# Kernel tuning notes

Measured on AMD Instinct MI355X. Metric: run time of the kernel, lower is better.

Reference implementation:

```python
import jax, jax.numpy as jnp
import numpy as np
from jax.scipy.special import logsumexp

HEAD = 12
EPS = 1.0


def _sinkhorn(dots):
    # dots: [b, h, n, n]. Faithful to the torch code: eps=1, max_iter=3,
    # update order u, v, u (the err<1e-6 early-break never triggers for
    # unconverged random-scale inputs, so we unroll the 3 iterations).
    C = -dots
    b, h, n, m = C.shape
    log_mu = -jnp.log(jnp.asarray(n, dtype=C.dtype))  # log(1/n)
    log_nu = -jnp.log(jnp.asarray(m, dtype=C.dtype))
    u = jnp.zeros((b, h, n), dtype=C.dtype)
    v = jnp.zeros((b, h, m), dtype=C.dtype)

    def M(u, v):
        # (-C + u_i + v_j) / eps
        return (-C + u[..., :, None] + v[..., None, :]) / EPS

    # i = 0: row update
    u = EPS * (log_mu - logsumexp(M(u, v), axis=-1)) + u
    # i = 1: column update (logsumexp over transpose == axis=-2)
    v = EPS * (log_nu - logsumexp(M(u, v), axis=-2)) + v
    # i = 2: row update
    u = EPS * (log_mu - logsumexp(M(u, v), axis=-1)) + u
    return jnp.exp(M(u, v))


def setup_inputs() -> dict:
    key = jax.random.key(0)
    ks = jax.random.split(key, 6)
    b, n, f = 8, 1024, 768
    x = jax.random.normal(ks[0], (b, n, f), dtype=jnp.float32)
    s = 1.0 / np.sqrt(f)
    Wq = jax.random.normal(ks[1], (f, f), dtype=jnp.float32) * s
    Wk = jax.random.normal(ks[2], (f, f), dtype=jnp.float32) * s
    Wv = jax.random.normal(ks[3], (f, f), dtype=jnp.float32) * s
    Wo = jax.random.normal(ks[4], (f, f), dtype=jnp.float32) * s
    bo = jax.random.normal(ks[5], (f,), dtype=jnp.float32) * 0.01
    return {"x": x, "Wq": Wq, "Wk": Wk, "Wv": Wv, "Wo": Wo, "bo": bo}


def reference(x, Wq, Wk, Wv, Wo, bo):
    b, n, f = x.shape
    h = HEAD
    d = f // h
    scale = d ** (-0.5)
    # nn.Linear: y = x @ W.T
    q = (x @ Wq.T).reshape(b, n, h, d).transpose(0, 2, 1, 3)  # [b,h,n,d]
    k = (x @ Wk.T).reshape(b, n, h, d).transpose(0, 2, 1, 3)
    v = (x @ Wv.T).reshape(b, n, h, d).transpose(0, 2, 1, 3)
    dots = jnp.einsum("bhid,bhjd->bhij", q, k) * scale  # [b,h,n,n]
    attn = _sinkhorn(dots)
    out = jnp.einsum("bhij,bhjd->bhid", attn, v)
    out = out.transpose(0, 2, 1, 3).reshape(b, n, f)
    return out @ Wo.T + bo
```

## Files before the change

kernel.cpp:

```cpp
#include <hip/hip_runtime.h>

#define DEV __device__ __forceinline__

typedef __attribute__((ext_vector_type(4))) float f32x4;
typedef __attribute__((ext_vector_type(16))) float f32x16;
typedef __attribute__((ext_vector_type(8))) short bf16x8;

DEV short f2bf(float f) {
    union { float f; unsigned u; } v; v.f = f;
    unsigned r = (v.u + 0x7fffu + ((v.u >> 16) & 1u)) >> 16;
    return (short)r;
}

#ifndef __has_builtin
#define __has_builtin(x) 0
#endif
#if __has_builtin(__builtin_amdgcn_cvt_pk_bf16_f32)
DEV unsigned pkbf(float a, float b) {
    auto r = __builtin_amdgcn_cvt_pk_bf16_f32(a, b);
    union { __typeof__(r) v; unsigned u; } u; u.v = r; return u.u;
}
#else
DEV unsigned pkbf(float a, float b) {
    return (unsigned)(unsigned short)f2bf(a) | ((unsigned)(unsigned short)f2bf(b) << 16);
}
#endif

DEV void gl_lds16(const void* g, void* l) {
    __builtin_amdgcn_global_load_lds(
        (__attribute__((address_space(1))) void*)(g),
        (__attribute__((address_space(3))) void*)(l), 16, 0, 0);
}

template <int ITERS>
DEV void stage_tile(const short* g, int ldg, short* lds, int t) {
    const int w = t >> 6;
#pragma unroll
    for (int it = 0; it < ITERS; ++it) {
        int row = it * 32 + (t >> 3);
        int cx = (t & 7) ^ ((t >> 3) & 7);
        gl_lds16(g + row * ldg + cx * 8, (char*)lds + it * 4096 + (w << 10));
    }
}

DEV bf16x8 ldfrag(const short* lds, int r, int kc) {
    return *(const bf16x8*)(lds + r * 64 + ((kc ^ (r & 7)) << 3));
}

__global__ void cvt_all(const float* __restrict__ x,
                        const float* __restrict__ wq, const float* __restrict__ wk,
                        const float* __restrict__ wv, const float* __restrict__ wo,
                        short* __restrict__ xb,
                        short* __restrict__ wqb, short* __restrict__ wkb,
                        short* __restrict__ wvb, short* __restrict__ wob) {
    int b = blockIdx.x;
    const float* s; short* d; int i;
    if (b < 6144) {
        s = x; d = xb; i = b * 256 + threadIdx.x;
    } else {
        int r = b - 6144;
        int wi = r / 576, rem = r - wi * 576;
        s = (wi == 0) ? wq : (wi == 1) ? wk : (wi == 2) ? wv : wo;
        d = (wi == 0) ? wqb : (wi == 1) ? wkb : (wi == 2) ? wvb : wob;
        i = rem * 256 + threadIdx.x;
    }
    float4 v = ((const float4*)s)[i];
    short4 o;
    o.x = f2bf(v.x); o.y = f2bf(v.y); o.z = f2bf(v.z); o.w = f2bf(v.w);
    ((short4*)d)[i] = o;
}

#define TSTRIDE 136
__global__ __launch_bounds__(256, 3) void proj_gemm(
    const short* __restrict__ xb,
    const short* __restrict__ wq, const short* __restrict__ wk, const short* __restrict__ wv,
    short* __restrict__ Qg, short* __restrict__ Kg, short* __restrict__ Vtg)
{
    __shared__ __align__(16) char smem[40960];
    short* const At = (short*)smem;
    short* const Bq = (short*)(smem + 16384);
    short* const Bk = (short*)(smem + 24576);
    short* const Bv = (short*)(smem + 32768);
    short* const Ct = (short*)smem;
    const int t = threadIdx.x;
    const int row0 = blockIdx.x * 128, col0 = blockIdx.y * 64;
    const int lane = t & 63, w = t >> 6;
    const int l31 = lane & 31, lh = lane >> 5;
    const int wm = w >> 1, wn = w & 1;

    f32x16 acc[3][2];
#pragma unroll
    for (int z = 0; z < 3; ++z)
#pragma unroll
        for (int tm = 0; tm < 2; ++tm) acc[z][tm] = (f32x16)(0.f);

    const short* Asrc = xb + (size_t)row0 * 768;
    const short* Qs = wq + (size_t)col0 * 768;
    const short* Ks = wk + (size_t)col0 * 768;
    const short* Vs = wv + (size_t)col0 * 768;

    for (int k = 0; k < 12; ++k) {
        __syncthreads();
        stage_tile<4>(Asrc + k * 64, 768, At, t);
        stage_tile<2>(Qs + k * 64, 768, Bq, t);
        stage_tile<2>(Ks + k * 64, 768, Bk, t);
        stage_tile<2>(Vs + k * 64, 768, Bv, t);
        __syncthreads();
#pragma unroll
        for (int s = 0; s < 4; ++s) {
            bf16x8 af[2];
#pragma unroll
            for (int tm = 0; tm < 2; ++tm) af[tm] = ldfrag(At, wm * 64 + tm * 32 + l31, s * 2 + lh);
            bf16x8 b0 = ldfrag(Bq, wn * 32 + l31, s * 2 + lh);
            bf16x8 b1 = ldfrag(Bk, wn * 32 + l31, s * 2 + lh);
            bf16x8 b2 = ldfrag(Bv, wn * 32 + l31, s * 2 + lh);
#pragma unroll
            for (int tm = 0; tm < 2; ++tm) {
                acc[0][tm] = __builtin_amdgcn_mfma_f32_32x32x16_bf16(af[tm], b0, acc[0][tm], 0, 0, 0);
                acc[1][tm] = __builtin_amdgcn_mfma_f32_32x32x16_bf16(af[tm], b1, acc[1][tm], 0, 0, 0);
                acc[2][tm] = __builtin_amdgcn_mfma_f32_32x32x16_bf16(af[tm], b2, acc[2][tm], 0, 0, 0);
            }
        }
    }
    __syncthreads();

    const int bb = row0 >> 10;
    const int head = bb * 12 + (col0 >> 6);

#pragma unroll
    for (int z = 0; z < 2; ++z) {
        const float sc = (z == 0) ? 0.125f * 1.4426950408889634f : 1.0f;
        const int ddl = wn * 32 + l31;
#pragma unroll
        for (int tm = 0; tm < 2; ++tm)
#pragma unroll
            for (int reg = 0; reg < 16; ++reg) {
                int rrl = wm * 64 + tm * 32 + (reg & 3) + 8 * (reg >> 2) + 4 * lh;
                Ct[rrl * TSTRIDE + ddl] = f2bf(acc[z][tm][reg] * sc);
            }
        __syncthreads();
        short* dst = (z == 0) ? Qg : Kg;
#pragma unroll
        for (int it = 0; it < 4; ++it) {
            int row = it * 32 + (t >> 3);
            int ck = t & 7;
            bf16x8 v = *(const bf16x8*)(Ct + row * TSTRIDE + ck * 8);
            int rr = (row0 & 1023) + row;
            *(bf16x8*)(dst + ((size_t)head * 1024 + rr) * 64 + ck * 8) = v;
        }
        __syncthreads();
    }

    {
        const int ddl = wn * 32 + l31;
#pragma unroll
        for (int tm = 0; tm < 2; ++tm)
#pragma unroll
            for (int g = 0; g < 4; ++g) {
                int rrl = wm * 64 + tm * 32 + 8 * g + 4 * lh;
                int j6 = rrl & 63;
                int pp = (rrl & ~63) | (j6 & 32) | ((j6 & 12) << 1) | ((j6 & 16) >> 2);
                short4 v4;
                v4.x = f2bf(acc[2][tm][4 * g + 0]);
                v4.y = f2bf(acc[2][tm][4 * g + 1]);
                v4.z = f2bf(acc[2][tm][4 * g + 2]);
                v4.w = f2bf(acc[2][tm][4 * g + 3]);
                *(short4*)(Ct + ddl * TSTRIDE + pp) = v4;
            }
        __syncthreads();
#pragma unroll
        for (int it = 0; it < 4; ++it) {
            int row = it * 16 + (t >> 4);
            int ck = t & 15;
            bf16x8 v = *(const bf16x8*)(Ct + row * TSTRIDE + ck * 8);
            *(bf16x8*)(Vtg + ((size_t)head * 64 + row) * 1024 + (row0 & 1023) + ck * 8) = v;
        }
    }
}

__global__ __launch_bounds__(256, 5) void lse_pass(
    const short* __restrict__ Aall, const short* __restrict__ Ball,
    const float* __restrict__ bias, float* __restrict__ outv,
    float bias_sign, float out_sign)
{
    __shared__ __align__(16) short At[64 * 64];
    __shared__ __align__(16) short Bt[128 * 64];
    __shared__ __align__(16) float biasl[1024];
    const int t = threadIdx.x;
    const int head = blockIdx.x % 96;
    const int r0 = (blockIdx.x / 96) * 64;
    const int lane = t & 63, w = t >> 6, quad = lane >> 4, c = lane & 15;
    const short* A = Aall + (size_t)head * 65536;
    const short* B = Ball + (size_t)head * 65536;

    stage_tile<2>(A + r0 * 64, 64, At, t);
    if (bias) {
        float4 v = ((const float4*)(bias + (size_t)head * 1024))[t];
        v.x *= bias_sign; v.y *= bias_sign; v.z *= bias_sign; v.w *= bias_sign;
        ((float4*)biasl)[t] = v;
    } else ((float4*)biasl)[t] = make_float4(0.f, 0.f, 0.f, 0.f);

    float lsum = 0.f;
    bf16x8 bfr[2];
    bool first = true;

    for (int j0 = 0; j0 < 1024; j0 += 128) {
        __syncthreads();
        stage_tile<4>(B + j0 * 64, 64, Bt, t);
        __syncthreads();
        if (first) {
#pragma unroll
            for (int ks = 0; ks < 2; ++ks) bfr[ks] = ldfrag(At, w * 16 + c, ks * 4 + quad);
            first = false;
        }
        f32x4 sacc[8];
#pragma unroll
        for (int fm = 0; fm < 8; ++fm) {
            float4 b4 = *(const float4*)(biasl + j0 + fm * 16 + quad * 4);
            sacc[fm] = (f32x4){b4.x, b4.y, b4.z, b4.w};
        }
#pragma unroll
        for (int ks = 0; ks < 2; ++ks) {
            bf16x8 af[8];
#pragma unroll
            for (int fm = 0; fm < 8; ++fm) af[fm] = ldfrag(Bt, fm * 16 + c, ks * 4 + quad);
#pragma unroll
            for (int fm = 0; fm < 8; ++fm)
                sacc[fm] = __builtin_amdgcn_mfma_f32_16x16x32_bf16(af[fm], bfr[ks], sacc[fm], 0, 0, 0);
        }
#pragma unroll
        for (int fm = 0; fm < 8; ++fm) {
            float p0 = __builtin_amdgcn_exp2f(sacc[fm][0]);
            float p1 = __builtin_amdgcn_exp2f(sacc[fm][1]);
            float p2 = __builtin_amdgcn_exp2f(sacc[fm][2]);
            float p3 = __builtin_amdgcn_exp2f(sacc[fm][3]);
            lsum += (p0 + p1) + (p2 + p3);
        }
    }

    lsum += __shfl_xor(lsum, 16);
    lsum += __shfl_xor(lsum, 32);
    if (quad == 0)
        outv[(size_t)head * 1024 + r0 + w * 16 + c] =
            out_sign * __builtin_amdgcn_logf(lsum);
}

__global__ __launch_bounds__(256, 4) void flash_pass(
    const short* __restrict__ Qall, const short* __restrict__ Kall,
    const short* __restrict__ Vtall, const float* __restrict__ v1,
    short* __restrict__ ctx)
{
    __shared__ __align__(16) short Qt[128 * 64];
    __shared__ __align__(16) short Kt[64 * 64];
    __shared__ __align__(16) short Vtl[64 * 64];
    __shared__ __align__(16) float v1l[1024];
    const int t = threadIdx.x;
    const int head = blockIdx.x % 96;
    const int r0 = (blockIdx.x / 96) * 128;
    const int lane = t & 63, w = t >> 6, quad = lane >> 4, c = lane & 15;
    const short* Q = Qall + (size_t)head * 65536;
    const short* K = Kall + (size_t)head * 65536;
    const short* Vt = Vtall + (size_t)head * 65536;

    stage_tile<4>(Q + r0 * 64, 64, Qt, t);
    ((float4*)v1l)[t] = ((const float4*)(v1 + (size_t)head * 1024))[t];

    float lsum[2] = {0.f, 0.f};
    f32x4 oacc[4][2];
#pragma unroll
    for (int md = 0; md < 4; ++md)
#pragma unroll
        for (int ni = 0; ni < 2; ++ni) oacc[md][ni] = (f32x4){0.f, 0.f, 0.f, 0.f};

    bf16x8 qfr[2][2];
    bool first = true;

    for (int j0 = 0; j0 < 1024; j0 += 64) {
        __syncthreads();
        stage_tile<2>(K + j0 * 64, 64, Kt, t);
        stage_tile<2>(Vt + j0, 1024, Vtl, t);
        __syncthreads();
        if (first) {
#pragma unroll
            for (int fn = 0; fn < 2; ++fn)
#pragma unroll
                for (int ks = 0; ks < 2; ++ks)
                    qfr[fn][ks] = ldfrag(Qt, w * 32 + fn * 16 + c, ks * 4 + quad);
            first = false;
        }
        f32x4 sacc[4][2];
#pragma unroll
        for (int fm = 0; fm < 4; ++fm) {
            float4 b4 = *(const float4*)(v1l + j0 + fm * 16 + quad * 4);
#pragma unroll
            for (int fn = 0; fn < 2; ++fn) sacc[fm][fn] = (f32x4){b4.x, b4.y, b4.z, b4.w};
        }
#pragma unroll
        for (int ks = 0; ks < 2; ++ks) {
            bf16x8 af[4];
#pragma unroll
            for (int fm = 0; fm < 4; ++fm) af[fm] = ldfrag(Kt, fm * 16 + c, ks * 4 + quad);
#pragma unroll
            for (int fm = 0; fm < 4; ++fm)
#pragma unroll
                for (int fn = 0; fn < 2; ++fn)
                    sacc[fm][fn] = __builtin_amdgcn_mfma_f32_16x16x32_bf16(af[fm], qfr[fn][ks], sacc[fm][fn], 0, 0, 0);
        }
        unsigned pk[4][2][2];
#pragma unroll
        for (int fm = 0; fm < 4; ++fm)
#pragma unroll
            for (int fn = 0; fn < 2; ++fn) {
                float p0 = __builtin_amdgcn_exp2f(sacc[fm][fn][0]);
                float p1 = __builtin_amdgcn_exp2f(sacc[fm][fn][1]);
                float p2 = __builtin_amdgcn_exp2f(sacc[fm][fn][2]);
                float p3 = __builtin_amdgcn_exp2f(sacc[fm][fn][3]);
                lsum[fn] += (p0 + p1) + (p2 + p3);
                pk[fm][fn][0] = pkbf(p0, p1);
                pk[fm][fn][1] = pkbf(p2, p3);
            }
#pragma unroll
        for (int ks = 0; ks < 2; ++ks) {
            bf16x8 vaf[4];
#pragma unroll
            for (int md = 0; md < 4; ++md) vaf[md] = ldfrag(Vtl, md * 16 + c, ks * 4 + quad);
#pragma unroll
            for (int ni = 0; ni < 2; ++ni) {
                union { bf16x8 v8; unsigned u4[4]; } b;
                b.u4[0] = pk[2 * ks + 0][ni][0];
                b.u4[1] = pk[2 * ks + 0][ni][1];
                b.u4[2] = pk[2 * ks + 1][ni][0];
                b.u4[3] = pk[2 * ks + 1][ni][1];
#pragma unroll
                for (int md = 0; md < 4; ++md)
                    oacc[md][ni] = __builtin_amdgcn_mfma_f32_16x16x32_bf16(vaf[md], b.v8, oacc[md][ni], 0, 0, 0);
            }
        }
    }

#pragma unroll
    for (int fn = 0; fn < 2; ++fn) {
        float s = lsum[fn];
        s += __shfl_xor(s, 16); s += __shfl_xor(s, 32);
        lsum[fn] = s;
    }
    const int bb = head / 12, hh = head % 12;
#pragma unroll
    for (int ni = 0; ni < 2; ++ni) {
        float nrm = __builtin_amdgcn_rcpf(1024.f * lsum[ni]);
        int rr = r0 + w * 32 + ni * 16 + c;
#pragma unroll
        for (int md = 0; md < 4; ++md) {
            short4 v4;
            v4.x = f2bf(oacc[md][ni][0] * nrm);
            v4.y = f2bf(oacc[md][ni][1] * nrm);
            v4.z = f2bf(oacc[md][ni][2] * nrm);
            v4.w = f2bf(oacc[md][ni][3] * nrm);
            *(short4*)(ctx + ((size_t)(bb * 1024 + rr)) * 768 + hh * 64 + md * 16 + quad * 4) = v4;
        }
    }
}

__global__ __launch_bounds__(256, 4) void out_gemm(
    const short* __restrict__ ctxb, const short* __restrict__ wo,
    const float* __restrict__ bo, float* __restrict__ out)
{
    __shared__ __align__(16) short At[128 * 64];
    __shared__ __align__(16) short Bt[128 * 64];
    const int t = threadIdx.x;
    const int row0 = blockIdx.x * 128, col0 = blockIdx.y * 128;
    const int lane = t & 63, w = t >> 6;
    const int l31 = lane & 31, lh = lane >> 5;
    const int wm = w >> 1, wn = w & 1;

    f32x16 acc[2][2];
#pragma unroll
    for (int i = 0; i < 2; ++i)
#pragma unroll
        for (int j = 0; j < 2; ++j) acc[i][j] = (f32x16)(0.f);

    for (int k0 = 0; k0 < 768; k0 += 64) {
        __syncthreads();
        stage_tile<4>(ctxb + (size_t)row0 * 768 + k0, 768, At, t);
        stage_tile<4>(wo + (size_t)col0 * 768 + k0, 768, Bt, t);
        __syncthreads();
#pragma unroll
        for (int s = 0; s < 4; ++s) {
            bf16x8 af[2], bfr[2];
#pragma unroll
            for (int tm = 0; tm < 2; ++tm) af[tm] = ldfrag(At, wm * 64 + tm * 32 + l31, s * 2 + lh);
#pragma unroll
            for (int tn = 0; tn < 2; ++tn) bfr[tn] = ldfrag(Bt, wn * 64 + tn * 32 + l31, s * 2 + lh);
#pragma unroll
            for (int tm = 0; tm < 2; ++tm)
#pragma unroll
                for (int tn = 0; tn < 2; ++tn)
                    acc[tm][tn] = __builtin_amdgcn_mfma_f32_32x32x16_bf16(af[tm], bfr[tn], acc[tm][tn], 0, 0, 0);
        }
    }
#pragma unroll
    for (int tm = 0; tm < 2; ++tm)
#pragma unroll
        for (int tn = 0; tn < 2; ++tn) {
            int gc = col0 + wn * 64 + tn * 32 + l31;
            float b = bo[gc];
#pragma unroll
            for (int reg = 0; reg < 16; ++reg) {
                int gr = row0 + wm * 64 + tm * 32 + (reg & 3) + 8 * (reg >> 2) + 4 * lh;
                out[(size_t)gr * 768 + gc] = acc[tm][tn][reg] + b;
            }
        }
}

extern "C" void kernel_launch(void* const* d_in, const int* in_sizes, int n_in,
                              void* d_out, int out_size, void* d_ws, size_t ws_size,
                              hipStream_t stream) {
    const float* x  = (const float*)d_in[0];
    const float* Wq = (const float*)d_in[1];
    const float* Wk = (const float*)d_in[2];
    const float* Wv = (const float*)d_in[3];
    const float* Wo = (const float*)d_in[4];
    const float* bo = (const float*)d_in[5];
    float* out = (float*)d_out;

    char* p = (char*)d_ws;
    short* xb  = (short*)p; p += (size_t)8192 * 768 * 2;
    short* wqb = (short*)p; p += (size_t)768 * 768 * 2;
    short* wkb = (short*)p; p += (size_t)768 * 768 * 2;
    short* wvb = (short*)p; p += (size_t)768 * 768 * 2;
    short* wob = (short*)p; p += (size_t)768 * 768 * 2;
    short* Qg  = (short*)p; p += (size_t)96 * 1024 * 64 * 2;
    short* Kg  = (short*)p; p += (size_t)96 * 1024 * 64 * 2;
    short* Vtg = (short*)p; p += (size_t)96 * 1024 * 64 * 2;
    float* r1  = (float*)p; p += (size_t)96 * 1024 * 4;
    float* v1  = (float*)p; p += (size_t)96 * 1024 * 4;
    short* ctx = (short*)p; p += (size_t)8192 * 768 * 2;

    cvt_all<<<6144 + 4 * 576, 256, 0, stream>>>(x, Wq, Wk, Wv, Wo, xb, wqb, wkb, wvb, wob);

    proj_gemm<<<dim3(64, 12), 256, 0, stream>>>(xb, wqb, wkb, wvb, Qg, Kg, Vtg);

    lse_pass<<<1536, 256, 0, stream>>>(Qg, Kg, nullptr, r1, 0.f, 1.f);
    lse_pass<<<1536, 256, 0, stream>>>(Kg, Qg, r1, v1, -1.f, -1.f);

    flash_pass<<<768, 256, 0, stream>>>(Qg, Kg, Vtg, v1, ctx);

    out_gemm<<<dim3(64, 6), 256, 0, stream>>>(ctx, wob, bo, out);
}
```

Baseline: 224.6 us.

## Switch attention passes to 32x32x16 MFMA and double LSE row tile

Rewrites lse_pass and flash_pass to use 32x32x16 bf16 MFMA instructions instead of 16x16x32, with one 32-row query tile per wave. lse_pass now processes 128 rows per block (half the grid) so each staged B tile is reused across more rows. The V^T permutation in proj_gemm is changed to match the new P-fragment layout for the PV MFMA. The aim is fewer LDS fragment loads per FLOP and fewer cross-lane reductions, at the cost of larger accumulators, lower lse occupancy and a smaller grid.

Measured after the change: 211.0 us. 6.1% less time.

```diff
diff --git a/kernel.cpp b/kernel.cpp
--- a/kernel.cpp
+++ b/kernel.cpp
@@ -158,8 +158,7 @@
 #pragma unroll
             for (int g = 0; g < 4; ++g) {
                 int rrl = wm * 64 + tm * 32 + 8 * g + 4 * lh;
-                int j6 = rrl & 63;
-                int pp = (rrl & ~63) | (j6 & 32) | ((j6 & 12) << 1) | ((j6 & 16) >> 2);
+                int pp = (rrl & ~12) | ((rrl & 8) >> 1) | ((rrl & 4) << 1);
                 short4 v4;
                 v4.x = f2bf(acc[2][tm][4 * g + 0]);
                 v4.y = f2bf(acc[2][tm][4 * g + 1]);
@@ -178,22 +177,23 @@
     }
 }
 
-__global__ __launch_bounds__(256, 5) void lse_pass(
+__global__ __launch_bounds__(256, 4) void lse_pass(
     const short* __restrict__ Aall, const short* __restrict__ Ball,
     const float* __restrict__ bias, float* __restrict__ outv,
     float bias_sign, float out_sign)
 {
-    __shared__ __align__(16) short At[64 * 64];
+    __shared__ __align__(16) short At[128 * 64];
     __shared__ __align__(16) short Bt[128 * 64];
     __shared__ __align__(16) float biasl[1024];
     const int t = threadIdx.x;
     const int head = blockIdx.x % 96;
-    const int r0 = (blockIdx.x / 96) * 64;
-    const int lane = t & 63, w = t >> 6, quad = lane >> 4, c = lane & 15;
+    const int r0 = (blockIdx.x / 96) * 128;
+    const int lane = t & 63, w = t >> 6;
+    const int l31 = lane & 31, lh = lane >> 5;
     const short* A = Aall + (size_t)head * 65536;
     const short* B = Ball + (size_t)head * 65536;
 
-    stage_tile<2>(A + r0 * 64, 64, At, t);
+    stage_tile<4>(A + r0 * 64, 64, At, t);
     if (bias) {
         float4 v = ((const float4*)(bias + (size_t)head * 1024))[t];
         v.x *= bias_sign; v.y *= bias_sign; v.z *= bias_sign; v.w *= bias_sign;
@@ -201,7 +201,7 @@
     } else ((float4*)biasl)[t] = make_float4(0.f, 0.f, 0.f, 0.f);
 
     float lsum = 0.f;
-    bf16x8 bfr[2];
+    bf16x8 bfr[4];
     bool first = true;
 
     for (int j0 = 0; j0 < 1024; j0 += 128) {
@@ -210,38 +210,42 @@
         __syncthreads();
         if (first) {
 #pragma unroll
-            for (int ks = 0; ks < 2; ++ks) bfr[ks] = ldfrag(At, w * 16 + c, ks * 4 + quad);
+            for (int s = 0; s < 4; ++s) bfr[s] = ldfrag(At, w * 32 + l31, s * 2 + lh);
             first = false;
         }
-        f32x4 sacc[8];
-#pragma unroll
-        for (int fm = 0; fm < 8; ++fm) {
-            float4 b4 = *(const float4*)(biasl + j0 + fm * 16 + quad * 4);
-            sacc[fm] = (f32x4){b4.x, b4.y, b4.z, b4.w};
-        }
-#pragma unroll
-        for (int ks = 0; ks < 2; ++ks) {
-            bf16x8 af[8];
-#pragma unroll
-            for (int fm = 0; fm < 8; ++fm) af[fm] = ldfrag(Bt, fm * 16 + c, ks * 4 + quad);
-#pragma unroll
-            for (int fm = 0; fm < 8; ++fm)
-                sacc[fm] = __builtin_amdgcn_mfma_f32_16x16x32_bf16(af[fm], bfr[ks], sacc[fm], 0, 0, 0);
-        }
-#pragma unroll
-        for (int fm = 0; fm < 8; ++fm) {
-            float p0 = __builtin_amdgcn_exp2f(sacc[fm][0]);
-            float p1 = __builtin_amdgcn_exp2f(sacc[fm][1]);
-            float p2 = __builtin_amdgcn_exp2f(sacc[fm][2]);
-            float p3 = __builtin_amdgcn_exp2f(sacc[fm][3]);
-            lsum += (p0 + p1) + (p2 + p3);
-        }
-    }
-
-    lsum += __shfl_xor(lsum, 16);
+        f32x16 sacc[4];
+#pragma unroll
+        for (int mt = 0; mt < 4; ++mt)
+#pragma unroll
+            for (int g = 0; g < 4; ++g) {
+                float4 b4 = *(const float4*)(biasl + j0 + mt * 32 + g * 8 + 4 * lh);
+                sacc[mt][4 * g + 0] = b4.x; sacc[mt][4 * g + 1] = b4.y;
+                sacc[mt][4 * g + 2] = b4.z; sacc[mt][4 * g + 3] = b4.w;
+            }
+#pragma unroll
+        for (int s = 0; s < 4; ++s) {
+            bf16x8 af[4];
+#pragma unroll
+            for (int mt = 0; mt < 4; ++mt) af[mt] = ldfrag(Bt, mt * 32 + l31, s * 2 + lh);
+#pragma unroll
+            for (int mt = 0; mt < 4; ++mt)
+                sacc[mt] = __builtin_amdgcn_mfma_f32_32x32x16_bf16(af[mt], bfr[s], sacc[mt], 0, 0, 0);
+        }
+#pragma unroll
+        for (int mt = 0; mt < 4; ++mt)
+#pragma unroll
+            for (int g = 0; g < 4; ++g) {
+                float p0 = __builtin_amdgcn_exp2f(sacc[mt][4 * g + 0]);
+                float p1 = __builtin_amdgcn_exp2f(sacc[mt][4 * g + 1]);
+                float p2 = __builtin_amdgcn_exp2f(sacc[mt][4 * g + 2]);
+                float p3 = __builtin_amdgcn_exp2f(sacc[mt][4 * g + 3]);
+                lsum += (p0 + p1) + (p2 + p3);
+            }
+    }
+
     lsum += __shfl_xor(lsum, 32);
-    if (quad == 0)
-        outv[(size_t)head * 1024 + r0 + w * 16 + c] =
+    if (lh == 0)
+        outv[(size_t)head * 1024 + r0 + w * 32 + l31] =
             out_sign * __builtin_amdgcn_logf(lsum);
 }
 
@@ -257,7 +261,8 @@
     const int t = threadIdx.x;
     const int head = blockIdx.x % 96;
     const int r0 = (blockIdx.x / 96) * 128;
-    const int lane = t & 63, w = t >> 6, quad = lane >> 4, c = lane & 15;
+    const int lane = t & 63, w = t >> 6;
+    const int l31 = lane & 31, lh = lane >> 5;
     const short* Q = Qall + (size_t)head * 65536;
     const short* K = Kall + (size_t)head * 65536;
     const short* Vt = Vtall + (size_t)head * 65536;
@@ -265,14 +270,12 @@
     stage_tile<4>(Q + r0 * 64, 64, Qt, t);
     ((float4*)v1l)[t] = ((const float4*)(v1 + (size_t)head * 1024))[t];
 
-    float lsum[2] = {0.f, 0.f};
-    f32x4 oacc[4][2];
-#pragma unroll
-    for (int md = 0; md < 4; ++md)
-#pragma unroll
-        for (int ni = 0; ni < 2; ++ni) oacc[md][ni] = (f32x4){0.f, 0.f, 0.f, 0.f};
-
-    bf16x8 qfr[2][2];
+    float lsum = 0.f;
+    f32x16 oacc[2];
+#pragma unroll
+    for (int md = 0; md < 2; ++md) oacc[md] = (f32x16)(0.f);
+
+    bf16x8 qfr[4];
     bool first = true;
 
     for (int j0 = 0; j0 < 1024; j0 += 64) {
@@ -282,83 +285,71 @@
         __syncthreads();
         if (first) {
 #pragma unroll
-            for (int fn = 0; fn < 2; ++fn)
-#pragma unroll
-                for (int ks = 0; ks < 2; ++ks)
-                    qfr[fn][ks] = ldfrag(Qt, w * 32 + fn * 16 + c, ks * 4 + quad);
+            for (int s = 0; s < 4; ++s) qfr[s] = ldfrag(Qt, w * 32 + l31, s * 2 + lh);
             first = false;
         }
-        f32x4 sacc[4][2];
-#pragma unroll
-        for (int fm = 0; fm < 4; ++fm) {
-            float4 b4 = *(const float4*)(v1l + j0 + fm * 16 + quad * 4);
-#pragma unroll
-            for (int fn = 0; fn < 2; ++fn) sacc[fm][fn] = (f32x4){b4.x, b4.y, b4.z, b4.w};
-        }
-#pragma unroll
-        for (int ks = 0; ks < 2; ++ks) {
-            bf16x8 af[4];
-#pragma unroll
-            for (int fm = 0; fm < 4; ++fm) af[fm] = ldfrag(Kt, fm * 16 + c, ks * 4 + quad);
-#pragma unroll
-            for (int fm = 0; fm < 4; ++fm)
-#pragma unroll
-                for (int fn = 0; fn < 2; ++fn)
-                    sacc[fm][fn] = __builtin_amdgcn_mfma_f32_16x16x32_bf16(af[fm], qfr[fn][ks], sacc[fm][fn], 0, 0, 0);
-        }
-        unsigned pk[4][2][2];
-#pragma unroll
-        for (int fm = 0; fm < 4; ++fm)
-#pragma unroll
-            for (int fn = 0; fn < 2; ++fn) {
-                float p0 = __builtin_amdgcn_exp2f(sacc[fm][fn][0]);
-                float p1 = __builtin_amdgcn_exp2f(sacc[fm][fn][1]);
-                float p2 = __builtin_amdgcn_exp2f(sacc[fm][fn][2]);
-                float p3 = __builtin_amdgcn_exp2f(sacc[fm][fn][3]);
-                lsum[fn] += (p0 + p1) + (p2 + p3);
-                pk[fm][fn][0] = pkbf(p0, p1);
-                pk[fm][fn][1] = pkbf(p2, p3);
-            }
-#pragma unroll
-        for (int ks = 0; ks < 2; ++ks) {
-            bf16x8 vaf[4];
-#pragma unroll
-            for (int md = 0; md < 4; ++md) vaf[md] = ldfrag(Vtl, md * 16 + c, ks * 4 + quad);
-#pragma unroll
-            for (int ni = 0; ni < 2; ++ni) {
-                union { bf16x8 v8; unsigned u4[4]; } b;
-                b.u4[0] = pk[2 * ks + 0][ni][0];
-                b.u4[1] = pk[2 * ks + 0][ni][1];
-                b.u4[2] = pk[2 * ks + 1][ni][0];
-                b.u4[3] = pk[2 * ks + 1][ni][1];
-#pragma unroll
-                for (int md = 0; md < 4; ++md)
-                    oacc[md][ni] = __builtin_amdgcn_mfma_f32_16x16x32_bf16(vaf[md], b.v8, oacc[md][ni], 0, 0, 0);
-            }
-        }
-    }
-
-#pragma unroll
-    for (int fn = 0; fn < 2; ++fn) {
-        float s = lsum[fn];
-        s += __shfl_xor(s, 16); s += __shfl_xor(s, 32);
-        lsum[fn] = s;
-    }
+        f32x16 sacc[2];
+#pragma unroll
+        for (int mt = 0; mt < 2; ++mt)
+#pragma unroll
+            for (int g = 0; g < 4; ++g) {
+                float4 b4 = *(const float4*)(v1l + j0 + mt * 32 + g * 8 + 4 * lh);
+                sacc[mt][4 * g + 0] = b4.x; sacc[mt][4 * g + 1] = b4.y;
+                sacc[mt][4 * g + 2] = b4.z; sacc[mt][4 * g + 3] = b4.w;
+            }
+#pragma unroll
+        for (int s = 0; s < 4; ++s) {
+            bf16x8 af[2];
+#pragma unroll
+            for (int mt = 0; mt < 2; ++mt) af[mt] = ldfrag(Kt, mt * 32 + l31, s * 2 + lh);
+#pragma unroll
+            for (int mt = 0; mt < 2; ++mt)
+                sacc[mt] = __builtin_amdgcn_mfma_f32_32x32x16_bf16(af[mt], qfr[s], sacc[mt], 0, 0, 0);
+        }
+        unsigned pkw[2][8];
+#pragma unroll
+        for (int mt = 0; mt < 2; ++mt)
+#pragma unroll
+            for (int g = 0; g < 4; ++g) {
+                float p0 = __builtin_amdgcn_exp2f(sacc[mt][4 * g + 0]);
+                float p1 = __builtin_amdgcn_exp2f(sacc[mt][4 * g + 1]);
+                float p2 = __builtin_amdgcn_exp2f(sacc[mt][4 * g + 2]);
+                float p3 = __builtin_amdgcn_exp2f(sacc[mt][4 * g + 3]);
+                lsum += (p0 + p1) + (p2 + p3);
+                pkw[mt][2 * g + 0] = pkbf(p0, p1);
+                pkw[mt][2 * g + 1] = pkbf(p2, p3);
+            }
+#pragma unroll
+        for (int q = 0; q < 4; ++q) {
+            union { bf16x8 v8; unsigned u4[4]; } b;
+            b.u4[0] = pkw[q >> 1][4 * (q & 1) + 0];
+            b.u4[1] = pkw[q >> 1][4 * (q & 1) + 1];
+            b.u4[2] = pkw[q >> 1][4 * (q & 1) + 2];
+            b.u4[3] = pkw[q >> 1][4 * (q & 1) + 3];
+#pragma unroll
+            for (int md = 0; md < 2; ++md) {
+                bf16x8 vaf = ldfrag(Vtl, md * 32 + l31, q * 2 + lh);
+                oacc[md] = __builtin_amdgcn_mfma_f32_32x32x16_bf16(vaf, b.v8, oacc[md], 0, 0, 0);
+            }
+        }
+    }
+
+    lsum += __shfl_xor(lsum, 32);
     const int bb = head / 12, hh = head % 12;
-#pragma unroll
-    for (int ni = 0; ni < 2; ++ni) {
-        float nrm = __builtin_amdgcn_rcpf(1024.f * lsum[ni]);
-        int rr = r0 + w * 32 + ni * 16 + c;
-#pragma unroll
-        for (int md = 0; md < 4; ++md) {
+    float nrm = __builtin_amdgcn_rcpf(1024.f * lsum);
+    int rr = r0 + w * 32 + l31;
+#pragma unroll
+    for (int md = 0; md < 2; ++md)
+#pragma unroll
+        for (int g = 0; g < 4; ++g) {
+            int d0 = md * 32 + g * 8 + 4 * lh;
             short4 v4;
-            v4.x = f2bf(oacc[md][ni][0] * nrm);
-            v4.y = f2bf(oacc[md][ni][1] * nrm);
-            v4.z = f2bf(oacc[md][ni][2] * nrm);
-            v4.w = f2bf(oacc[md][ni][3] * nrm);
-            *(short4*)(ctx + ((size_t)(bb * 1024 + rr)) * 768 + hh * 64 + md * 16 + quad * 4) = v4;
-        }
-    }
+            v4.x = f2bf(oacc[md][4 * g + 0] * nrm);
+            v4.y = f2bf(oacc[md][4 * g + 1] * nrm);
+            v4.z = f2bf(oacc[md][4 * g + 2] * nrm);
+            v4.w = f2bf(oacc[md][4 * g + 3] * nrm);
+            *(short4*)(ctx + ((size_t)(bb * 1024 + rr)) * 768 + hh * 64 + d0) = v4;
+        }
 }
 
 __global__ __launch_bounds__(256, 4) void out_gemm(
@@ -440,8 +431,8 @@
 
     proj_gemm<<<dim3(64, 12), 256, 0, stream>>>(xb, wqb, wkb, wvb, Qg, Kg, Vtg);
 
-    lse_pass<<<1536, 256, 0, stream>>>(Qg, Kg, nullptr, r1, 0.f, 1.f);
-    lse_pass<<<1536, 256, 0, stream>>>(Kg, Qg, r1, v1, -1.f, -1.f);
+    lse_pass<<<768, 256, 0, stream>>>(Qg, Kg, nullptr, r1, 0.f, 1.f);
+    lse_pass<<<768, 256, 0, stream>>>(Kg, Qg, r1, v1, -1.f, -1.f);
 
     flash_pass<<<768, 256, 0, stream>>>(Qg, Kg, Vtg, v1, ctx);
 
```

## Use 32x32 MFMA with larger row tiles in LSE pass; compute row sums via MFMA

Applied to the files above, without the earlier changes.

The logsumexp pass switches from 16x16x32 to 32x32x16 bf16 MFMA and doubles the rows per block to 128, halving the grid and cutting repeated B-tile staging and LDS fragment loads per output. The flash pass drops its scalar per-row exp sum and cross-lane shuffles, and instead gets the row sums from an extra MFMA that multiplies the packed bf16 probabilities by a ones vector. This moves VALU adds onto the matrix units. The trade-off is that the sums now come from bf16-rounded probabilities, and the lse kernel uses more registers and LDS, so its launch bound occupancy drops from 5 to 4.

Measured after the change: 214.1 us. -4.7%, faster.

```diff
diff --git a/kernel.cpp b/kernel.cpp
--- a/kernel.cpp
+++ b/kernel.cpp
@@ -178,22 +178,23 @@
     }
 }
 
-__global__ __launch_bounds__(256, 5) void lse_pass(
+__global__ __launch_bounds__(256, 4) void lse_pass(
     const short* __restrict__ Aall, const short* __restrict__ Ball,
     const float* __restrict__ bias, float* __restrict__ outv,
     float bias_sign, float out_sign)
 {
-    __shared__ __align__(16) short At[64 * 64];
+    __shared__ __align__(16) short At[128 * 64];
     __shared__ __align__(16) short Bt[128 * 64];
     __shared__ __align__(16) float biasl[1024];
     const int t = threadIdx.x;
     const int head = blockIdx.x % 96;
-    const int r0 = (blockIdx.x / 96) * 64;
-    const int lane = t & 63, w = t >> 6, quad = lane >> 4, c = lane & 15;
+    const int r0 = (blockIdx.x / 96) * 128;
+    const int lane = t & 63, w = t >> 6;
+    const int l31 = lane & 31, lh = lane >> 5;
     const short* A = Aall + (size_t)head * 65536;
     const short* B = Ball + (size_t)head * 65536;
 
-    stage_tile<2>(A + r0 * 64, 64, At, t);
+    stage_tile<4>(A + r0 * 64, 64, At, t);
     if (bias) {
         float4 v = ((const float4*)(bias + (size_t)head * 1024))[t];
         v.x *= bias_sign; v.y *= bias_sign; v.z *= bias_sign; v.w *= bias_sign;
@@ -201,7 +202,7 @@
     } else ((float4*)biasl)[t] = make_float4(0.f, 0.f, 0.f, 0.f);
 
     float lsum = 0.f;
-    bf16x8 bfr[2];
+    bf16x8 bfr[4];
     bool first = true;
 
     for (int j0 = 0; j0 < 1024; j0 += 128) {
@@ -210,38 +211,42 @@
         __syncthreads();
         if (first) {
 #pragma unroll
-            for (int ks = 0; ks < 2; ++ks) bfr[ks] = ldfrag(At, w * 16 + c, ks * 4 + quad);
+            for (int s = 0; s < 4; ++s) bfr[s] = ldfrag(At, w * 32 + l31, s * 2 + lh);
             first = false;
         }
-        f32x4 sacc[8];
-#pragma unroll
-        for (int fm = 0; fm < 8; ++fm) {
-            float4 b4 = *(const float4*)(biasl + j0 + fm * 16 + quad * 4);
-            sacc[fm] = (f32x4){b4.x, b4.y, b4.z, b4.w};
-        }
-#pragma unroll
-        for (int ks = 0; ks < 2; ++ks) {
-            bf16x8 af[8];
-#pragma unroll
-            for (int fm = 0; fm < 8; ++fm) af[fm] = ldfrag(Bt, fm * 16 + c, ks * 4 + quad);
-#pragma unroll
-            for (int fm = 0; fm < 8; ++fm)
-                sacc[fm] = __builtin_amdgcn_mfma_f32_16x16x32_bf16(af[fm], bfr[ks], sacc[fm], 0, 0, 0);
-        }
-#pragma unroll
-        for (int fm = 0; fm < 8; ++fm) {
-            float p0 = __builtin_amdgcn_exp2f(sacc[fm][0]);
-            float p1 = __builtin_amdgcn_exp2f(sacc[fm][1]);
-            float p2 = __builtin_amdgcn_exp2f(sacc[fm][2]);
-            float p3 = __builtin_amdgcn_exp2f(sacc[fm][3]);
-            lsum += (p0 + p1) + (p2 + p3);
-        }
-    }
-
-    lsum += __shfl_xor(lsum, 16);
+        f32x16 sacc[4];
+#pragma unroll
+        for (int mt = 0; mt < 4; ++mt)
+#pragma unroll
+            for (int g = 0; g < 4; ++g) {
+                float4 b4 = *(const float4*)(biasl + j0 + mt * 32 + g * 8 + 4 * lh);
+                sacc[mt][4 * g + 0] = b4.x; sacc[mt][4 * g + 1] = b4.y;
+                sacc[mt][4 * g + 2] = b4.z; sacc[mt][4 * g + 3] = b4.w;
+            }
+#pragma unroll
+        for (int s = 0; s < 4; ++s) {
+            bf16x8 af[4];
+#pragma unroll
+            for (int mt = 0; mt < 4; ++mt) af[mt] = ldfrag(Bt, mt * 32 + l31, s * 2 + lh);
+#pragma unroll
+            for (int mt = 0; mt < 4; ++mt)
+                sacc[mt] = __builtin_amdgcn_mfma_f32_32x32x16_bf16(af[mt], bfr[s], sacc[mt], 0, 0, 0);
+        }
+#pragma unroll
+        for (int mt = 0; mt < 4; ++mt)
+#pragma unroll
+            for (int g = 0; g < 4; ++g) {
+                float p0 = __builtin_amdgcn_exp2f(sacc[mt][4 * g + 0]);
+                float p1 = __builtin_amdgcn_exp2f(sacc[mt][4 * g + 1]);
+                float p2 = __builtin_amdgcn_exp2f(sacc[mt][4 * g + 2]);
+                float p3 = __builtin_amdgcn_exp2f(sacc[mt][4 * g + 3]);
+                lsum += (p0 + p1) + (p2 + p3);
+            }
+    }
+
     lsum += __shfl_xor(lsum, 32);
-    if (quad == 0)
-        outv[(size_t)head * 1024 + r0 + w * 16 + c] =
+    if (lh == 0)
+        outv[(size_t)head * 1024 + r0 + w * 32 + l31] =
             out_sign * __builtin_amdgcn_logf(lsum);
 }
 
@@ -265,12 +270,18 @@
     stage_tile<4>(Q + r0 * 64, 64, Qt, t);
     ((float4*)v1l)[t] = ((const float4*)(v1 + (size_t)head * 1024))[t];
 
-    float lsum[2] = {0.f, 0.f};
     f32x4 oacc[4][2];
+    f32x4 lsacc[2];
 #pragma unroll
     for (int md = 0; md < 4; ++md)
 #pragma unroll
         for (int ni = 0; ni < 2; ++ni) oacc[md][ni] = (f32x4){0.f, 0.f, 0.f, 0.f};
+#pragma unroll
+    for (int ni = 0; ni < 2; ++ni) lsacc[ni] = (f32x4){0.f, 0.f, 0.f, 0.f};
+
+    bf16x8 ones;
+#pragma unroll
+    for (int i = 0; i < 8; ++i) ones[i] = (short)0x3F80;
 
     bf16x8 qfr[2][2];
     bool first = true;
@@ -315,7 +326,6 @@
                 float p1 = __builtin_amdgcn_exp2f(sacc[fm][fn][1]);
                 float p2 = __builtin_amdgcn_exp2f(sacc[fm][fn][2]);
                 float p3 = __builtin_amdgcn_exp2f(sacc[fm][fn][3]);
-                lsum[fn] += (p0 + p1) + (p2 + p3);
                 pk[fm][fn][0] = pkbf(p0, p1);
                 pk[fm][fn][1] = pkbf(p2, p3);
             }
@@ -334,20 +344,15 @@
 #pragma unroll
                 for (int md = 0; md < 4; ++md)
                     oacc[md][ni] = __builtin_amdgcn_mfma_f32_16x16x32_bf16(vaf[md], b.v8, oacc[md][ni], 0, 0, 0);
-            }
-        }
-    }
-
-#pragma unroll
-    for (int fn = 0; fn < 2; ++fn) {
-        float s = lsum[fn];
-        s += __shfl_xor(s, 16); s += __shfl_xor(s, 32);
-        lsum[fn] = s;
-    }
+                lsacc[ni] = __builtin_amdgcn_mfma_f32_16x16x32_bf16(ones, b.v8, lsacc[ni], 0, 0, 0);
+            }
+        }
+    }
+
     const int bb = head / 12, hh = head % 12;
 #pragma unroll
     for (int ni = 0; ni < 2; ++ni) {
-        float nrm = __builtin_amdgcn_rcpf(1024.f * lsum[ni]);
+        float nrm = __builtin_amdgcn_rcpf(1024.f * lsacc[ni][0]);
         int rr = r0 + w * 32 + ni * 16 + c;
 #pragma unroll
         for (int md = 0; md < 4; ++md) {
@@ -440,8 +445,8 @@
 
     proj_gemm<<<dim3(64, 12), 256, 0, stream>>>(xb, wqb, wkb, wvb, Qg, Kg, Vtg);
 
-    lse_pass<<<1536, 256, 0, stream>>>(Qg, Kg, nullptr, r1, 0.f, 1.f);
-    lse_pass<<<1536, 256, 0, stream>>>(Kg, Qg, r1, v1, -1.f, -1.f);
+    lse_pass<<<768, 256, 0, stream>>>(Qg, Kg, nullptr, r1, 0.f, 1.f);
+    lse_pass<<<768, 256, 0, stream>>>(Kg, Qg, r1, v1, -1.f, -1.f);
 
     flash_pass<<<768, 256, 0, stream>>>(Qg, Kg, Vtg, v1, ctx);
 
```
